# Optimization experiments

Hardware: AMD Instinct MI355X
Metric: run time of the kernel (lower is better)

The kernel has to match this reference:

```python
import jax, jax.numpy as jnp
import numpy as np

DECAY = 0.9


def setup_inputs() -> dict:
    key = jax.random.key(0)
    k1, k2 = jax.random.split(key)
    x = jax.random.normal(k1, (8, 2048, 512), dtype=jnp.float32)
    key_embed = jax.random.normal(k2, (8, 2048, 64), dtype=jnp.float32)
    return {"x": x, "key_embed": key_embed, "key_optim": 1}


def reference(x, key_embed, key_optim):
    # key_embed: [h, c, d]
    h, c, d = key_embed.shape
    b, t, _ = x.shape
    x = x.astype(jnp.float32)
    # 'b t (h d) -> h b t d'
    xh = x.reshape(b, t, h, d).transpose(2, 0, 1, 3)  # [h, b, t, d]
    flat = xh.reshape(h, b * t, d)                     # [h, n, d]

    # nearest codebook entry: argmax(-cdist) == argmin of squared distance
    x_sq = jnp.sum(flat * flat, axis=-1, keepdims=True)           # [h, n, 1]
    e_sq = jnp.sum(key_embed * key_embed, axis=-1)[:, None, :]    # [h, 1, c]
    dots = jnp.einsum('hnd,hcd->hnc', flat, key_embed)            # [h, n, c]
    d2 = x_sq - 2.0 * dots + e_sq
    ind = jnp.argmin(d2, axis=-1)                                 # [h, n]
    emb_ind = ind.reshape(h, b, t)                                # [h, b, t]

    # gather quantized vectors: [h, b, t, d]
    head_idx = jnp.arange(h)[:, None, None]
    quantized = key_embed[head_idx, emb_ind]

    # EMA codebook update: key_embed.lerp_(emb_sum, decay)
    emb_sum = jnp.zeros_like(key_embed).at[jnp.arange(h)[:, None], ind].add(flat)
    if key_optim:
        new_key_embed = key_embed + DECAY * (emb_sum - key_embed)
    else:
        new_key_embed = key_embed

    # 'h b t d -> b t (h d)'
    quant_out = quantized.transpose(1, 2, 0, 3).reshape(b, t, h * d)
    # 'h b n -> b n h'
    emb_ind_out = emb_ind.transpose(1, 2, 0)
    return (quant_out, emb_ind_out, new_key_embed)
```

## Files before the change

kernel.cpp:

```cpp
#include <hip/hip_runtime.h>
#include <float.h>

#define H   8
#define C   2048
#define D   64
#define NPH 16384
#define HD  512
#define DECAYF 0.9f
#define DELTA 3.0f
#define CAP 64
#define VB  256

typedef __attribute__((ext_vector_type(8))) short short8v;
typedef __attribute__((ext_vector_type(4))) float f32x4;

__device__ inline unsigned short f32_to_bf16_rne(float f) {
    unsigned int x = __float_as_uint(f);
    return (unsigned short)((x + 0x7FFFu + ((x >> 16) & 1u)) >> 16);
}

__global__ __launch_bounds__(256) void vq_prep_kernel(const float* __restrict__ ke,
                                                      unsigned short* __restrict__ keb2,
                                                      float* __restrict__ esq) {
    const int row = blockIdx.x * 256 + threadIdx.x;
    const int c   = row & 15;
    const int ch  = (row >> 4) & 127;
    const int h   = row >> 11;
    const float* e = ke + (size_t)row * D;
    unsigned short* kb = keb2 + ((size_t)h * C * D) + (size_t)ch * 1024;
#pragma unroll
    for (int kf = 0; kf < 2; ++kf)
#pragma unroll
        for (int g = 0; g < 4; ++g) {
            float4 v0 = ((const float4*)e)[kf * 8 + g * 2];
            float4 v1 = ((const float4*)e)[kf * 8 + g * 2 + 1];
            short8v o;
            o[0] = (short)f32_to_bf16_rne(v0.x); o[1] = (short)f32_to_bf16_rne(v0.y);
            o[2] = (short)f32_to_bf16_rne(v0.z); o[3] = (short)f32_to_bf16_rne(v0.w);
            o[4] = (short)f32_to_bf16_rne(v1.x); o[5] = (short)f32_to_bf16_rne(v1.y);
            o[6] = (short)f32_to_bf16_rne(v1.z); o[7] = (short)f32_to_bf16_rne(v1.w);
            *(short8v*)(kb + kf * 512 + (g * 16 + c) * 8) = o;
        }
    float s = 0.f;
#pragma unroll
    for (int d = 0; d < D; ++d) s = fmaf(e[d], e[d], s);
    esq[row] = s;
}

__global__ __launch_bounds__(256, 2)
void vq_main_kernel(const float* __restrict__ x,
                    const unsigned short* __restrict__ keb2,
                    const float* __restrict__ ke,
                    const float* __restrict__ esq,
                    float* __restrict__ outq,
                    float* __restrict__ outi,
                    unsigned short* __restrict__ indw,
                    unsigned int* __restrict__ counts) {
    __shared__ int            ccnt[VB];
    __shared__ unsigned short cand[VB][CAP];
    __shared__ int            sidx[VB];

    const int tid  = threadIdx.x;
    const int lane = tid & 63;
    const int w    = __builtin_amdgcn_readfirstlane(tid >> 6);
    const int h    = blockIdx.x & 7;
    const int n0   = (blockIdx.x >> 3) * VB;

    const unsigned short* keb2h = keb2 + (size_t)h * C * D;
    const float* keh  = ke  + (size_t)h * C * D;
    const float* esqh = esq + (size_t)h * C;

    ccnt[tid] = 0;
    __syncthreads();

    const int col = lane & 15;
    const int kg  = (lane >> 4) * 8;

    short8v afr[4][2];
#pragma unroll
    for (int vt = 0; vt < 4; ++vt) {
        const float* xp = x + (size_t)(n0 + w * 64 + vt * 16 + col) * HD
                            + (size_t)h * D + kg;
#pragma unroll
        for (int kf = 0; kf < 2; ++kf) {
            float4 u0 = *(const float4*)(xp + kf * 32);
            float4 u1 = *(const float4*)(xp + kf * 32 + 4);
            short8v a;
            a[0] = (short)f32_to_bf16_rne(u0.x); a[1] = (short)f32_to_bf16_rne(u0.y);
            a[2] = (short)f32_to_bf16_rne(u0.z); a[3] = (short)f32_to_bf16_rne(u0.w);
            a[4] = (short)f32_to_bf16_rne(u1.x); a[5] = (short)f32_to_bf16_rne(u1.y);
            a[6] = (short)f32_to_bf16_rne(u1.z); a[7] = (short)f32_to_bf16_rne(u1.w);
            afr[vt][kf] = a;
        }
    }

    float amin[16];
#pragma unroll
    for (int s = 0; s < 16; ++s) amin[s] = FLT_MAX;

#define LOADB2(CH, B0, B1, EQ)                                                 \
    {                                                                          \
        const short8v* kb = (const short8v*)(keb2h + (size_t)(CH) * 1024);     \
        B0 = kb[lane];                                                         \
        B1 = kb[64 + lane];                                                    \
        EQ = esqh[((CH) << 4) + col];                                          \
    }

#define STEP1(C0V, C1V, QV)                                                    \
    {                                                                          \
        _Pragma("unroll")                                                      \
        for (int vt = 0; vt < 4; ++vt) {                                       \
            f32x4 acc = {0.f, 0.f, 0.f, 0.f};                                  \
            acc = __builtin_amdgcn_mfma_f32_16x16x32_bf16(afr[vt][0], C0V, acc, 0, 0, 0); \
            acc = __builtin_amdgcn_mfma_f32_16x16x32_bf16(afr[vt][1], C1V, acc, 0, 0, 0); \
            _Pragma("unroll")                                                  \
            for (int r = 0; r < 4; ++r) {                                      \
                float sc = fmaf(-2.f, acc[r], QV);                             \
                amin[vt * 4 + r] = fminf(amin[vt * 4 + r], sc);                \
            }                                                                  \
        }                                                                      \
    }

#define STEP2(C0V, C1V, QV, CB)                                                \
    {                                                                          \
        _Pragma("unroll")                                                      \
        for (int vt = 0; vt < 4; ++vt) {                                       \
            f32x4 acc = {0.f, 0.f, 0.f, 0.f};                                  \
            acc = __builtin_amdgcn_mfma_f32_16x16x32_bf16(afr[vt][0], C0V, acc, 0, 0, 0); \
            acc = __builtin_amdgcn_mfma_f32_16x16x32_bf16(afr[vt][1], C1V, acc, 0, 0, 0); \
            _Pragma("unroll")                                                  \
            for (int r = 0; r < 4; ++r) {                                      \
                float sc = fmaf(-2.f, acc[r], QV);                             \
                if (sc <= amin[vt * 4 + r] + DELTA) {                          \
                    const int vec = w * 64 + vt * 16 + ((lane >> 4) << 2) + r; \
                    int pos = atomicAdd(&ccnt[vec], 1);                        \
                    if (pos < CAP) cand[vec][pos] = (unsigned short)((CB) + col); \
                }                                                              \
            }                                                                  \
        }                                                                      \
    }

    {
        short8v s0a, s0b, s1a, s1b, s2a, s2b, s3a, s3b;
        float   q0, q1, q2, q3;
        LOADB2(0, s0a, s0b, q0);
        LOADB2(1, s1a, s1b, q1);
        LOADB2(2, s2a, s2b, q2);
        LOADB2(3, s3a, s3b, q3);
#pragma unroll 1
        for (int g = 0; g < 32; ++g) {
            {
                short8v c0 = s0a, c1 = s0b; float q = q0;
                LOADB2((4 * g + 4) & 127, s0a, s0b, q0);
                STEP1(c0, c1, q);
            }
            {
                short8v c0 = s1a, c1 = s1b; float q = q1;
                LOADB2((4 * g + 5) & 127, s1a, s1b, q1);
                STEP1(c0, c1, q);
            }
            {
                short8v c0 = s2a, c1 = s2b; float q = q2;
                LOADB2((4 * g + 6) & 127, s2a, s2b, q2);
                STEP1(c0, c1, q);
            }
            {
                short8v c0 = s3a, c1 = s3b; float q = q3;
                LOADB2((4 * g + 7) & 127, s3a, s3b, q3);
                STEP1(c0, c1, q);
            }
        }
    }

#pragma unroll
    for (int s = 0; s < 16; ++s) {
        float v = amin[s];
        v = fminf(v, __shfl_xor(v, 1));
        v = fminf(v, __shfl_xor(v, 2));
        v = fminf(v, __shfl_xor(v, 4));
        v = fminf(v, __shfl_xor(v, 8));
        amin[s] = v;
    }

    {
        short8v s0a, s0b, s1a, s1b, s2a, s2b, s3a, s3b;
        float   q0, q1, q2, q3;
        LOADB2(0, s0a, s0b, q0);
        LOADB2(1, s1a, s1b, q1);
        LOADB2(2, s2a, s2b, q2);
        LOADB2(3, s3a, s3b, q3);
#pragma unroll 1
        for (int g = 0; g < 32; ++g) {
            {
                short8v c0 = s0a, c1 = s0b; float q = q0;
                LOADB2((4 * g + 4) & 127, s0a, s0b, q0);
                STEP2(c0, c1, q, (4 * g + 0) << 4);
            }
            {
                short8v c0 = s1a, c1 = s1b; float q = q1;
                LOADB2((4 * g + 5) & 127, s1a, s1b, q1);
                STEP2(c0, c1, q, (4 * g + 1) << 4);
            }
            {
                short8v c0 = s2a, c1 = s2b; float q = q2;
                LOADB2((4 * g + 6) & 127, s2a, s2b, q2);
                STEP2(c0, c1, q, (4 * g + 2) << 4);
            }
            {
                short8v c0 = s3a, c1 = s3b; float q = q3;
                LOADB2((4 * g + 7) & 127, s3a, s3b, q3);
                STEP2(c0, c1, q, (4 * g + 3) << 4);
            }
        }
    }
    __syncthreads();

    {
        const float4* xr = (const float4*)(x + (size_t)(n0 + tid) * HD + (size_t)h * D);
        const int nc = ccnt[tid];
        float bb = FLT_MAX;
        int   bi = 0x7fffffff;
        if (nc <= CAP) {
            for (int i = 0; i < nc; ++i) {
                const int code = cand[tid][i];
                const float4* er = (const float4*)(keh + (size_t)code * D);
                float s = 0.f;
#pragma unroll 4
                for (int kq = 0; kq < 16; ++kq) {
                    float4 a4 = xr[kq]; float4 e4 = er[kq];
                    s = fmaf(a4.x, e4.x, s); s = fmaf(a4.y, e4.y, s);
                    s = fmaf(a4.z, e4.z, s); s = fmaf(a4.w, e4.w, s);
                }
                float sc = fmaf(-2.f, s, esqh[code]);
                if (sc < bb || (sc == bb && code < bi)) { bb = sc; bi = code; }
            }
        } else {
            for (int code = 0; code < C; ++code) {
                const float4* er = (const float4*)(keh + (size_t)code * D);
                float s = 0.f;
#pragma unroll 4
                for (int kq = 0; kq < 16; ++kq) {
                    float4 a4 = xr[kq]; float4 e4 = er[kq];
                    s = fmaf(a4.x, e4.x, s); s = fmaf(a4.y, e4.y, s);
                    s = fmaf(a4.z, e4.z, s); s = fmaf(a4.w, e4.w, s);
                }
                float sc = fmaf(-2.f, s, esqh[code]);
                if (sc < bb) { bb = sc; bi = code; }
            }
        }
        sidx[tid] = bi;
        outi[(size_t)(n0 + tid) * H + h] = (float)bi;
        indw[((size_t)h << 14) + n0 + tid] = (unsigned short)bi;
        atomicAdd(&counts[(h << 11) + bi], 1u);
    }
    __syncthreads();

#pragma unroll
    for (int ii = 0; ii < 2; ++ii) {
        const int v  = ii * 128 + (tid >> 1);
        const int db = (tid & 1) * 32;
        const int ci = sidx[v];
        const float* ev = keh + (size_t)ci * D + db;
        float* qo = outq + (size_t)(n0 + v) * HD + (size_t)h * D + db;
#pragma unroll
        for (int i = 0; i < 8; ++i)
            ((float4*)qo)[i] = ((const float4*)ev)[i];
    }
}

__global__ __launch_bounds__(256) void vq_scan_kernel(const unsigned int* __restrict__ counts,
                                                      unsigned int* __restrict__ off,
                                                      unsigned int* __restrict__ cur) {
    __shared__ unsigned int sa[C], sb[C];
    const int h   = blockIdx.x;
    const int tid = threadIdx.x;
#pragma unroll
    for (int j = 0; j < 8; ++j) sa[j * 256 + tid] = counts[(h << 11) + j * 256 + tid];
    __syncthreads();
    unsigned int* src = sa;
    unsigned int* dst = sb;
    for (int s = 1; s < C; s <<= 1) {
#pragma unroll
        for (int j = 0; j < 8; ++j) {
            const int c = j * 256 + tid;
            unsigned int v = src[c];
            if (c >= s) v += src[c - s];
            dst[c] = v;
        }
        __syncthreads();
        unsigned int* t = src; src = dst; dst = t;
    }
#pragma unroll
    for (int j = 0; j < 8; ++j) {
        const int c = j * 256 + tid;
        const unsigned int e = c ? src[c - 1] : 0u;
        off[(h << 11) + c] = e;
        cur[(h << 11) + c] = e;
    }
}

__global__ __launch_bounds__(256) void vq_scatter_kernel(const unsigned short* __restrict__ ind,
                                                         unsigned int* __restrict__ cur,
                                                         unsigned int* __restrict__ perm) {
    const int g = blockIdx.x * 256 + threadIdx.x;
    const int h = g >> 14;
    const int n = g & 16383;
    const int c = ind[g];
    const unsigned int pos = atomicAdd(&cur[(h << 11) + c], 1u);
    perm[((size_t)h << 14) + pos] = (unsigned int)n;
}

__global__ __launch_bounds__(256) void vq_reduce_kernel(const float* __restrict__ x,
                                                        const float* __restrict__ ke,
                                                        const unsigned int* __restrict__ perm,
                                                        const unsigned int* __restrict__ counts,
                                                        const unsigned int* __restrict__ off,
                                                        const int* __restrict__ ko,
                                                        float* __restrict__ outk) {
    __shared__ double sred[3][64];
    const int tid  = threadIdx.x;
    const int lane = tid & 63;
    const int w    = tid >> 6;
    const int pair = blockIdx.x;
    const int h    = pair >> 11;

    const unsigned int cnt = counts[pair];
    const unsigned int o   = off[pair];
    const unsigned int* pl = perm + ((size_t)h << 14) + o;
    const float* xh = x + (size_t)h * D;

    double a0 = 0.0, a1 = 0.0, a2 = 0.0, a3 = 0.0;
    unsigned int i = (unsigned int)w;
    for (; i + 12 < cnt; i += 16) {
        const unsigned int v0 = pl[i], v1 = pl[i + 4], v2 = pl[i + 8], v3 = pl[i + 12];
        a0 += (double)xh[(size_t)v0 * HD + lane];
        a1 += (double)xh[(size_t)v1 * HD + lane];
        a2 += (double)xh[(size_t)v2 * HD + lane];
        a3 += (double)xh[(size_t)v3 * HD + lane];
    }
    for (; i < cnt; i += 4)
        a0 += (double)xh[(size_t)pl[i] * HD + lane];
    const double part = ((a0 + a1) + a2) + a3;

    if (w) sred[w - 1][lane] = part;
    __syncthreads();
    if (w == 0) {
        const double acc = ((part + sred[0][lane]) + sred[1][lane]) + sred[2][lane];
        const float esum = (float)acc;
        const float kv   = ke[(size_t)pair * D + lane];
        const float ov   = ko[0] ? (kv + DECAYF * (esum - kv)) : kv;
        outk[(size_t)pair * D + lane] = ov;
    }
}

extern "C" void kernel_launch(void* const* d_in, const int* in_sizes, int n_in,
                              void* d_out, int out_size, void* d_ws, size_t ws_size,
                              hipStream_t stream) {
    const float* x  = (const float*)d_in[0];
    const float* ke = (const float*)d_in[1];
    const int*   ko = (const int*)d_in[2];

    float* out  = (float*)d_out;
    float* outq = out;
    float* outi = out + (size_t)H * NPH * D;
    float* outk = outi + (size_t)NPH * H;

    float*          esq    = (float*)d_ws;
    unsigned short* keb2   = (unsigned short*)(esq + H * C);
    unsigned short* indw   = keb2 + (size_t)H * C * D;
    unsigned int*   counts = (unsigned int*)(indw + (size_t)H * NPH);
    unsigned int*   offv   = counts + H * C;
    unsigned int*   curv   = offv + H * C;
    unsigned int*   perm   = curv + H * C;

    hipMemsetAsync(counts, 0, (size_t)H * C * sizeof(unsigned int), stream);

    vq_prep_kernel<<<(H * C) / 256, 256, 0, stream>>>(ke, keb2, esq);
    vq_main_kernel<<<512, 256, 0, stream>>>(x, keb2, ke, esq, outq, outi, indw, counts);
    vq_scan_kernel<<<H, 256, 0, stream>>>(counts, offv, curv);
    vq_scatter_kernel<<<512, 256, 0, stream>>>(indw, curv, perm);
    vq_reduce_kernel<<<H * C, 256, 0, stream>>>(x, ke, perm, counts, offv, ko, outk);
}
```

Before: 208.6 us.

## Interleave independent MFMA chains across two codebook chunks and raise occupancy

The distance loops now issue eight independent MFMA accumulators covering two codebook chunks back to back, instead of dependent pairs per vector tile. The epilogue min/threshold work is deferred until after both chunks' MFMAs, with s_setprio raised around the MFMA bursts. Launch bounds go from 2 to 4 blocks per CU to hide latency. Together these aim to remove MFMA dependency stalls and interleave epilogues across waves. The higher occupancy target caps VGPRs, which could cause spills given the many live accumulators.

```diff
diff --git a/kernel.cpp b/kernel.cpp
--- a/kernel.cpp
+++ b/kernel.cpp
@@ -47,7 +47,7 @@
     esq[row] = s;
 }
 
-__global__ __launch_bounds__(256, 2)
+__global__ __launch_bounds__(256, 4)
 void vq_main_kernel(const float* __restrict__ x,
                     const unsigned short* __restrict__ keb2,
                     const float* __restrict__ ke,
@@ -106,31 +106,41 @@
         EQ = esqh[((CH) << 4) + col];                                          \
     }
 
-#define STEP1(C0V, C1V, QV)                                                    \
+#define MFMA4(C0V, C1V, A0, A1, A2, A3)                                        \
+    {                                                                          \
+        A0 = (f32x4){0.f, 0.f, 0.f, 0.f};                                      \
+        A1 = (f32x4){0.f, 0.f, 0.f, 0.f};                                      \
+        A2 = (f32x4){0.f, 0.f, 0.f, 0.f};                                      \
+        A3 = (f32x4){0.f, 0.f, 0.f, 0.f};                                      \
+        A0 = __builtin_amdgcn_mfma_f32_16x16x32_bf16(afr[0][0], C0V, A0, 0, 0, 0); \
+        A1 = __builtin_amdgcn_mfma_f32_16x16x32_bf16(afr[1][0], C0V, A1, 0, 0, 0); \
+        A2 = __builtin_amdgcn_mfma_f32_16x16x32_bf16(afr[2][0], C0V, A2, 0, 0, 0); \
+        A3 = __builtin_amdgcn_mfma_f32_16x16x32_bf16(afr[3][0], C0V, A3, 0, 0, 0); \
+        A0 = __builtin_amdgcn_mfma_f32_16x16x32_bf16(afr[0][1], C1V, A0, 0, 0, 0); \
+        A1 = __builtin_amdgcn_mfma_f32_16x16x32_bf16(afr[1][1], C1V, A1, 0, 0, 0); \
+        A2 = __builtin_amdgcn_mfma_f32_16x16x32_bf16(afr[2][1], C1V, A2, 0, 0, 0); \
+        A3 = __builtin_amdgcn_mfma_f32_16x16x32_bf16(afr[3][1], C1V, A3, 0, 0, 0); \
+    }
+
+#define EPI1(A0, A1, A2, A3, QV)                                               \
+    {                                                                          \
+        _Pragma("unroll")                                                      \
+        for (int r = 0; r < 4; ++r) {                                          \
+            amin[0 + r]  = fminf(amin[0 + r],  fmaf(-2.f, A0[r], QV));         \
+            amin[4 + r]  = fminf(amin[4 + r],  fmaf(-2.f, A1[r], QV));         \
+            amin[8 + r]  = fminf(amin[8 + r],  fmaf(-2.f, A2[r], QV));         \
+            amin[12 + r] = fminf(amin[12 + r], fmaf(-2.f, A3[r], QV));         \
+        }                                                                      \
+    }
+
+#define EPI2(A0, A1, A2, A3, QV, CB)                                           \
     {                                                                          \
         _Pragma("unroll")                                                      \
         for (int vt = 0; vt < 4; ++vt) {                                       \
-            f32x4 acc = {0.f, 0.f, 0.f, 0.f};                                  \
-            acc = __builtin_amdgcn_mfma_f32_16x16x32_bf16(afr[vt][0], C0V, acc, 0, 0, 0); \
-            acc = __builtin_amdgcn_mfma_f32_16x16x32_bf16(afr[vt][1], C1V, acc, 0, 0, 0); \
+            const f32x4 aa = (vt == 0) ? A0 : (vt == 1) ? A1 : (vt == 2) ? A2 : A3; \
             _Pragma("unroll")                                                  \
             for (int r = 0; r < 4; ++r) {                                      \
-                float sc = fmaf(-2.f, acc[r], QV);                             \
-                amin[vt * 4 + r] = fminf(amin[vt * 4 + r], sc);                \
-            }                                                                  \
-        }                                                                      \
-    }
-
-#define STEP2(C0V, C1V, QV, CB)                                                \
-    {                                                                          \
-        _Pragma("unroll")                                                      \
-        for (int vt = 0; vt < 4; ++vt) {                                       \
-            f32x4 acc = {0.f, 0.f, 0.f, 0.f};                                  \
-            acc = __builtin_amdgcn_mfma_f32_16x16x32_bf16(afr[vt][0], C0V, acc, 0, 0, 0); \
-            acc = __builtin_amdgcn_mfma_f32_16x16x32_bf16(afr[vt][1], C1V, acc, 0, 0, 0); \
-            _Pragma("unroll")                                                  \
-            for (int r = 0; r < 4; ++r) {                                      \
-                float sc = fmaf(-2.f, acc[r], QV);                             \
+                float sc = fmaf(-2.f, aa[r], QV);                              \
                 if (sc <= amin[vt * 4 + r] + DELTA) {                          \
                     const int vec = w * 64 + vt * 16 + ((lane >> 4) << 2) + r; \
                     int pos = atomicAdd(&ccnt[vec], 1);                        \
@@ -147,27 +157,32 @@
         LOADB2(1, s1a, s1b, q1);
         LOADB2(2, s2a, s2b, q2);
         LOADB2(3, s3a, s3b, q3);
+        f32x4 xA0, xA1, xA2, xA3, yA0, yA1, yA2, yA3;
 #pragma unroll 1
         for (int g = 0; g < 32; ++g) {
             {
-                short8v c0 = s0a, c1 = s0b; float q = q0;
+                short8v c0 = s0a, c1 = s0b; float qa = q0;
+                short8v d0 = s1a, d1 = s1b; float qb = q1;
                 LOADB2((4 * g + 4) & 127, s0a, s0b, q0);
-                STEP1(c0, c1, q);
+                LOADB2((4 * g + 5) & 127, s1a, s1b, q1);
+                __builtin_amdgcn_s_setprio(1);
+                MFMA4(c0, c1, xA0, xA1, xA2, xA3);
+                MFMA4(d0, d1, yA0, yA1, yA2, yA3);
+                __builtin_amdgcn_s_setprio(0);
+                EPI1(xA0, xA1, xA2, xA3, qa);
+                EPI1(yA0, yA1, yA2, yA3, qb);
             }
             {
-                short8v c0 = s1a, c1 = s1b; float q = q1;
-                LOADB2((4 * g + 5) & 127, s1a, s1b, q1);
-                STEP1(c0, c1, q);
-            }
-            {
-                short8v c0 = s2a, c1 = s2b; float q = q2;
+                short8v c0 = s2a, c1 = s2b; float qa = q2;
+                short8v d0 = s3a, d1 = s3b; float qb = q3;
                 LOADB2((4 * g + 6) & 127, s2a, s2b, q2);
-                STEP1(c0, c1, q);
-            }
-            {
-                short8v c0 = s3a, c1 = s3b; float q = q3;
                 LOADB2((4 * g + 7) & 127, s3a, s3b, q3);
-                STEP1(c0, c1, q);
+                __builtin_amdgcn_s_setprio(1);
+                MFMA4(c0, c1, xA0, xA1, xA2, xA3);
+                MFMA4(d0, d1, yA0, yA1, yA2, yA3);
+                __builtin_amdgcn_s_setprio(0);
+                EPI1(xA0, xA1, xA2, xA3, qa);
+                EPI1(yA0, yA1, yA2, yA3, qb);
             }
         }
     }
@@ -189,27 +204,32 @@
         LOADB2(1, s1a, s1b, q1);
         LOADB2(2, s2a, s2b, q2);
         LOADB2(3, s3a, s3b, q3);
+        f32x4 xA0, xA1, xA2, xA3, yA0, yA1, yA2, yA3;
 #pragma unroll 1
         for (int g = 0; g < 32; ++g) {
             {
-                short8v c0 = s0a, c1 = s0b; float q = q0;
+                short8v c0 = s0a, c1 = s0b; float qa = q0;
+                short8v d0 = s1a, d1 = s1b; float qb = q1;
                 LOADB2((4 * g + 4) & 127, s0a, s0b, q0);
-                STEP2(c0, c1, q, (4 * g + 0) << 4);
+                LOADB2((4 * g + 5) & 127, s1a, s1b, q1);
+                __builtin_amdgcn_s_setprio(1);
+                MFMA4(c0, c1, xA0, xA1, xA2, xA3);
+                MFMA4(d0, d1, yA0, yA1, yA2, yA3);
+                __builtin_amdgcn_s_setprio(0);
+                EPI2(xA0, xA1, xA2, xA3, qa, (4 * g + 0) << 4);
+                EPI2(yA0, yA1, yA2, yA3, qb, (4 * g + 1) << 4);
             }
             {
-                short8v c0 = s1a, c1 = s1b; float q = q1;
-                LOADB2((4 * g + 5) & 127, s1a, s1b, q1);
-                STEP2(c0, c1, q, (4 * g + 1) << 4);
-            }
-            {
-                short8v c0 = s2a, c1 = s2b; float q = q2;
+                short8v c0 = s2a, c1 = s2b; float qa = q2;
+                short8v d0 = s3a, d1 = s3b; float qb = q3;
                 LOADB2((4 * g + 6) & 127, s2a, s2b, q2);
-                STEP2(c0, c1, q, (4 * g + 2) << 4);
-            }
-            {
-                short8v c0 = s3a, c1 = s3b; float q = q3;
                 LOADB2((4 * g + 7) & 127, s3a, s3b, q3);
-                STEP2(c0, c1, q, (4 * g + 3) << 4);
+                __builtin_amdgcn_s_setprio(1);
+                MFMA4(c0, c1, xA0, xA1, xA2, xA3);
+                MFMA4(d0, d1, yA0, yA1, yA2, yA3);
+                __builtin_amdgcn_s_setprio(0);
+                EPI2(xA0, xA1, xA2, xA3, qa, (4 * g + 2) << 4);
+                EPI2(yA0, yA1, yA2, yA3, qb, (4 * g + 3) << 4);
             }
         }
     }
```

Result: slower. 310.9 us (+49.0%).
